# Kernel tuning notes

Hardware: AMD Instinct MI355X
Metric: run time of the kernel (lower is better)

The kernel has to match this reference:

```python
import jax, jax.numpy as jnp
import numpy as np

DIM = 1024
NUM_HEADS = 16
HEAD_DIM = DIM // NUM_HEADS
SCALE = HEAD_DIM ** -0.5
B, N = 4, 2048


def setup_inputs() -> dict:
    key = jax.random.key(0)
    ks = jax.random.split(key, 5)
    s = 1.0 / np.sqrt(DIM)  # ~ torch Linear init scale
    x = jax.random.normal(ks[0], (B, N, DIM), dtype=jnp.float32)
    Wq = jax.random.normal(ks[1], (DIM, DIM), dtype=jnp.float32) * s
    Wk = jax.random.normal(ks[2], (DIM, DIM), dtype=jnp.float32) * s
    Wv = jax.random.normal(ks[3], (DIM, DIM), dtype=jnp.float32) * s
    Wo = jax.random.normal(ks[4], (DIM, DIM), dtype=jnp.float32) * s
    mask = jnp.tril(jnp.ones((N, N), dtype=bool))  # causal 2D bool mask
    return {"x": x, "mask": mask, "Wq": Wq, "Wk": Wk, "Wv": Wv, "Wo": Wo}


def reference(x, mask, Wq, Wk, Wv, Wo):
    Bb, Nn, D = x.shape
    def split_heads(t):
        return t.reshape(Bb, Nn, NUM_HEADS, HEAD_DIM).transpose(0, 2, 1, 3)  # [B,H,N,d]
    q = split_heads(x @ Wq.T)
    k = split_heads(x @ Wk.T)
    v = split_heads(x @ Wv.T)
    attn = jnp.einsum('bhqd,bhkd->bhqk', q, k) * SCALE  # [B,H,N,N]
    # 2D mask -> broadcast over batch and heads; ~mask positions set to -inf
    attn = jnp.where(mask[None, None, :, :], attn, -jnp.inf)
    attn = jax.nn.softmax(attn, axis=-1)
    out = jnp.einsum('bhqk,bhkd->bhqd', attn, v)
    out = out.transpose(0, 2, 1, 3).reshape(Bb, Nn, D)
    return out @ Wo.T
```

## Files before the change

### kernel.cpp

```cpp
#include <hip/hip_runtime.h>
#include <stdint.h>

#define Bq   4
#define Nseq 2048
#define NH   16
#define HD   64
#define DIMD 1024

typedef float  f32x4   __attribute__((ext_vector_type(4)));
typedef float  f32x16  __attribute__((ext_vector_type(16)));
typedef __bf16 bf16x8  __attribute__((ext_vector_type(8)));
typedef short  s16x4   __attribute__((ext_vector_type(4)));

typedef __attribute__((address_space(1))) void as1_void;
typedef __attribute__((address_space(3))) void as3_void;

static __device__ __forceinline__ uint16_t f2bf(float f) {
    uint32_t u = __builtin_bit_cast(uint32_t, f);
    u += 0x7fffu + ((u >> 16) & 1u);
    return (uint16_t)(u >> 16);
}

static __device__ __forceinline__ uint32_t pk2(float a, float b) {
    uint32_t ua = __builtin_bit_cast(uint32_t, a);
    uint32_t ub = __builtin_bit_cast(uint32_t, b);
    return (ua >> 16) | (ub & 0xffff0000u);
}

static __device__ __forceinline__ void asyncLoad16(const uint16_t* g, uint16_t* l) {
    __builtin_amdgcn_global_load_lds((as1_void*)g, (as3_void*)l, 16, 0, 0);
}

static __device__ __forceinline__ void storeOut(float* p, float v)    { *p = v; }
static __device__ __forceinline__ void storeOut(uint16_t* p, float v) { *p = f2bf(v); }

__global__ void cast_all(const float* __restrict__ x,
                         const float* __restrict__ wq, const float* __restrict__ wk,
                         const float* __restrict__ wv, const float* __restrict__ wo,
                         uint16_t* __restrict__ dst) {
    size_t i = ((size_t)blockIdx.x * blockDim.x + threadIdx.x) * 4;
    const float* src; size_t off; float scale = 1.0f;
    if (i < 8388608) { src = x; off = i; }
    else {
        size_t wI = i - 8388608;
        size_t wi = wI >> 20;
        off = wI & 1048575;
        src = (wi == 0) ? wq : (wi == 1) ? wk : (wi == 2) ? wv : wo;
        if (wi == 0) scale = 0.18033688011112042f;
    }
    float4 v = *(const float4*)(src + off);
    ushort4 o;
    o.x = f2bf(v.x * scale); o.y = f2bf(v.y * scale);
    o.z = f2bf(v.z * scale); o.w = f2bf(v.w * scale);
    *(ushort4*)(dst + i) = o;
}

template <typename OutT>
__global__ __launch_bounds__(256) void gemm_bt(
    const uint16_t* __restrict__ A, const uint16_t* __restrict__ W0,
    OutT* __restrict__ C0, int K, int Nld, int blocksPerSec,
    size_t wSecStride, size_t cSecStride, uint16_t* __restrict__ vtb, int vSec)
{
    __shared__ __align__(16) uint16_t As[128*64];
    __shared__ __align__(16) uint16_t Bs[128*64];

    const int t = threadIdx.x, lane = t & 63, w = t >> 6;
    const int wr = w >> 1, wc = w & 1;
    const int half = lane >> 5, ml = lane & 31;

    const int m0  = blockIdx.x * 128;
    const int sec = blockIdx.y / blocksPerSec;
    const int n0  = (blockIdx.y % blocksPerSec) * 128;
    const uint16_t* Wp = W0 + (size_t)sec * wSecStride;
    OutT* C = C0 + (size_t)sec * cSecStride;

    int srow[4], sg[4];
    #pragma unroll
    for (int i = 0; i < 4; ++i) {
        int s = t + 256*i;
        srow[i] = s >> 3;
        sg[i]   = (s & 7) ^ (srow[i] & 7);
    }

    int arow[2], brow[2];
    #pragma unroll
    for (int i = 0; i < 2; ++i) {
        arow[i] = wr*64 + i*32 + ml;
        brow[i] = wc*64 + i*32 + ml;
    }

    f32x16 acc[2][2] = {};

    for (int k0 = 0; k0 < K; k0 += 64) {
        __syncthreads();
        #pragma unroll
        for (int i = 0; i < 4; ++i) {
            asyncLoad16(A  + (size_t)(m0 + srow[i])*K + k0 + sg[i]*8,
                        As + (size_t)(w*64 + 256*i)*8);
            asyncLoad16(Wp + (size_t)(n0 + srow[i])*K + k0 + sg[i]*8,
                        Bs + (size_t)(w*64 + 256*i)*8);
        }
        __syncthreads();

        #pragma unroll
        for (int s = 0; s < 4; ++s) {
            const int chunk = s*2 + half;
            bf16x8 af[2], bfr[2];
            #pragma unroll
            for (int i = 0; i < 2; ++i) {
                int m = arow[i];
                af[i]  = *(const bf16x8*)(As + (size_t)(m*8 + (chunk ^ (m & 7)))*8);
                int n = brow[i];
                bfr[i] = *(const bf16x8*)(Bs + (size_t)(n*8 + (chunk ^ (n & 7)))*8);
            }
            #pragma unroll
            for (int mt = 0; mt < 2; ++mt)
                #pragma unroll
                for (int nt = 0; nt < 2; ++nt)
                    acc[mt][nt] = __builtin_amdgcn_mfma_f32_32x32x16_bf16(
                        af[mt], bfr[nt], acc[mt][nt], 0, 0, 0);
        }
    }

    if (vtb != nullptr && sec == vSec) {
        #pragma unroll
        for (int mt = 0; mt < 2; ++mt)
            #pragma unroll
            for (int nt = 0; nt < 2; ++nt) {
                int colg = n0 + wc*64 + nt*32 + ml;
                int hh = colg >> 6, dd = colg & 63;
                #pragma unroll
                for (int g = 0; g < 4; ++g) {
                    int rowg = m0 + wr*64 + mt*32 + 8*g + 4*half;
                    int bb = rowg >> 11, nn = rowg & 2047;
                    ushort4 o4;
                    o4.x = f2bf(acc[mt][nt][4*g + 0]);
                    o4.y = f2bf(acc[mt][nt][4*g + 1]);
                    o4.z = f2bf(acc[mt][nt][4*g + 2]);
                    o4.w = f2bf(acc[mt][nt][4*g + 3]);
                    *(ushort4*)(vtb + ((size_t)((bb*NH + hh)*HD + dd))*Nseq + nn) = o4;
                }
            }
    } else {
        #pragma unroll
        for (int mt = 0; mt < 2; ++mt)
            #pragma unroll
            for (int nt = 0; nt < 2; ++nt) {
                int col = n0 + wc*64 + nt*32 + ml;
                #pragma unroll
                for (int r = 0; r < 16; ++r) {
                    int row = m0 + wr*64 + mt*32 + (r & 3) + 8*(r >> 2) + 4*half;
                    storeOut(&C[(size_t)row * Nld + col], acc[mt][nt][r]);
                }
            }
    }
}

__global__ __launch_bounds__(256, 4) void attn(
    const uint16_t* __restrict__ Q, const uint16_t* __restrict__ K,
    const uint16_t* __restrict__ Vt, uint16_t* __restrict__ O)
{
    __shared__ __align__(16) uint16_t Kb[2][64*64];
    __shared__ __align__(16) uint16_t Vb[2][64*64];

    const int t = threadIdx.x, lane = t & 63, w = t >> 6;
    const int quad = lane >> 4, c = lane & 15;
    const int y = blockIdx.y;
    const int qi = (y < 4) ? (15 - y) : (y < 8) ? (y + 4) : (y < 12) ? (y - 4) : (15 - y);
    const int q0 = qi * 128;
    const int bh = blockIdx.x, b = bh >> 4, h = bh & 15;
    const size_t tokBase = (size_t)b * Nseq;
    const int hcol = h * HD;
    uint16_t* Qs = (uint16_t*)Kb;

    #define STAGE_KV(k0_, buf_)                                             \
        _Pragma("unroll")                                                    \
        for (int i = 0; i < 2; ++i) {                                        \
            int s = t + 256*i;                                               \
            int row = s >> 3, gg = (s & 7) ^ (row & 7);                      \
            asyncLoad16(K + (tokBase + (k0_) + row)*DIMD + hcol + gg*8,      \
                        Kb[buf_] + (size_t)(w*64 + 256*i)*8);                \
            asyncLoad16(Vt + ((size_t)bh*HD + row)*Nseq + (k0_) + gg*8,      \
                        Vb[buf_] + (size_t)(w*64 + 256*i)*8);                \
        }

    #pragma unroll
    for (int i = 0; i < 4; ++i) {
        int s = t + 256*i;
        int row = s >> 3, gg = (s & 7) ^ (row & 7);
        asyncLoad16(Q + (tokBase + q0 + row)*DIMD + hcol + gg*8,
                    Qs + (size_t)(w*64 + 256*i)*8);
    }
    __syncthreads();
    bf16x8 qf[2][2];
    #pragma unroll
    for (int qt = 0; qt < 2; ++qt)
        #pragma unroll
        for (int ks = 0; ks < 2; ++ks) {
            int row = w*32 + qt*16 + c;
            int pos = (ks*4 + quad) ^ (row & 7);
            qf[qt][ks] = *(const bf16x8*)(Qs + (size_t)(row*8 + pos)*8);
        }
    __syncthreads();
    STAGE_KV(0, 0);

    const int wrow0 = q0 + w*32;
    const int end = 2*qi + 2;
    f32x4  o[2][4] = {};
    float  l_lane[2] = {0.f, 0.f};

    for (int kt = 0; kt < end; ++kt) {
        const int cur = kt & 1, nxt = cur ^ 1;
        const int k0 = kt * 64;
        __syncthreads();

        if (kt + 1 < end) { STAGE_KV((kt+1)*64, nxt); }

        if (k0 > wrow0 + 31) continue;

        const uint16_t* Ks = Kb[cur];
        const uint16_t* Vs = Vb[cur];

        f32x4 sv[2][4] = {};
        #pragma unroll
        for (int nt = 0; nt < 4; ++nt)
            #pragma unroll
            for (int ks = 0; ks < 2; ++ks) {
                int row = nt*16 + c;
                int pos = (ks*4 + quad) ^ (row & 7);
                bf16x8 kf = *(const bf16x8*)(Ks + (size_t)(row*8 + pos)*8);
                sv[0][nt] = __builtin_amdgcn_mfma_f32_16x16x32_bf16(kf, qf[0][ks], sv[0][nt], 0, 0, 0);
                sv[1][nt] = __builtin_amdgcn_mfma_f32_16x16x32_bf16(kf, qf[1][ks], sv[1][nt], 0, 0, 0);
            }

        if (k0 + 63 > wrow0) {
            #pragma unroll
            for (int qt = 0; qt < 2; ++qt)
                #pragma unroll
                for (int nt = 0; nt < 4; ++nt)
                    #pragma unroll
                    for (int r = 0; r < 4; ++r) {
                        int kvg = k0 + nt*16 + quad*4 + r;
                        int qg  = wrow0 + qt*16 + c;
                        if (kvg > qg) sv[qt][nt][r] = -340.0f;
                    }
        }

        s16x4 pb[2][4];
        #pragma unroll
        for (int qt = 0; qt < 2; ++qt)
            #pragma unroll
            for (int nt = 0; nt < 4; ++nt) {
                float p0 = __builtin_amdgcn_exp2f(sv[qt][nt][0]);
                float p1 = __builtin_amdgcn_exp2f(sv[qt][nt][1]);
                float p2 = __builtin_amdgcn_exp2f(sv[qt][nt][2]);
                float p3 = __builtin_amdgcn_exp2f(sv[qt][nt][3]);
                l_lane[qt] += (p0 + p1) + (p2 + p3);
                union { uint32_t u[2]; s16x4 v; } pu;
                pu.u[0] = pk2(p0, p1);
                pu.u[1] = pk2(p2, p3);
                pb[qt][nt] = pu.v;
            }

        #pragma unroll
        for (int s4 = 0; s4 < 4; ++s4)
            #pragma unroll
            for (int dt = 0; dt < 4; ++dt) {
                int row = dt*16 + c;
                int chunk = s4*2 + (quad >> 1);
                int pos = chunk ^ (row & 7);
                s16x4 vf = *(const s16x4*)(Vs + (size_t)(row*8 + pos)*8 + (quad & 1)*4);
                o[0][dt] = __builtin_amdgcn_mfma_f32_16x16x16bf16_1k(vf, pb[0][s4], o[0][dt], 0, 0, 0);
                o[1][dt] = __builtin_amdgcn_mfma_f32_16x16x16bf16_1k(vf, pb[1][s4], o[1][dt], 0, 0, 0);
            }
    }

    #pragma unroll
    for (int qt = 0; qt < 2; ++qt) {
        float l = l_lane[qt];
        l += __shfl_xor(l, 16);
        l += __shfl_xor(l, 32);
        float inv = 1.0f / l;
        int tok = (int)(q0 + w*32 + qt*16 + c);
        #pragma unroll
        for (int dt = 0; dt < 4; ++dt) {
            ushort4 o4;
            o4.x = f2bf(o[qt][dt][0] * inv);
            o4.y = f2bf(o[qt][dt][1] * inv);
            o4.z = f2bf(o[qt][dt][2] * inv);
            o4.w = f2bf(o[qt][dt][3] * inv);
            *(ushort4*)(O + (tokBase + tok)*DIMD + hcol + dt*16 + quad*4) = o4;
        }
    }
    #undef STAGE_KV
}

extern "C" void kernel_launch(void* const* d_in, const int* in_sizes, int n_in,
                              void* d_out, int out_size, void* d_ws, size_t ws_size,
                              hipStream_t stream) {
    const float* x  = (const float*)d_in[0];
    const float* Wq = (const float*)d_in[2];
    const float* Wk = (const float*)d_in[3];
    const float* Wv = (const float*)d_in[4];
    const float* Wo = (const float*)d_in[5];

    uint16_t* ws  = (uint16_t*)d_ws;
    uint16_t* xb  = ws;
    uint16_t* wqb = ws + 8388608;
    uint16_t* wob = wqb + 3*1048576;
    uint16_t* qb  = ws + 12582912;
    uint16_t* kb  = qb + 8388608;
    uint16_t* vtb = kb + 8388608;
    uint16_t* ab  = xb;

    cast_all<<<12288, 256, 0, stream>>>(x, Wq, Wk, Wv, Wo, ws);

    gemm_bt<uint16_t><<<dim3(64, 24), 256, 0, stream>>>(
        xb, wqb, qb, DIMD, DIMD, 8, (size_t)1048576, (size_t)8388608, vtb, 2);

    attn<<<dim3(64, 16), 256, 0, stream>>>(qb, kb, vtb, ab);

    gemm_bt<float><<<dim3(64, 8), 256, 0, stream>>>(
        ab, wob, (float*)d_out, DIMD, DIMD, 8, (size_t)0, (size_t)0, nullptr, -1);
}
```

Before: 248.4 us.

## Add 256x256-tile double-buffered QKV GEMM with interleaved async prefetch

Replaces the 128x128 QKV projection GEMM with a new 512-thread kernel that computes 256x256 output tiles. It double-buffers A and B in LDS with async global-to-LDS loads spread between MFMA phases, and uses explicit barriers and s_setprio to overlap loads with compute. The larger tile raises arithmetic intensity and cuts global traffic, but the kernel uses 128KB of LDS and launches only 384 blocks, so occupancy and tail balance are at risk. The V section still writes a transposed layout, now as ushort4 stores.

```diff
diff --git a/kernel.cpp b/kernel.cpp
--- a/kernel.cpp
+++ b/kernel.cpp
@@ -55,6 +55,152 @@
     *(ushort4*)(dst + i) = o;
 }
 
+#define BAR()    asm volatile("s_barrier" ::: "memory")
+#define VMBAR(N) asm volatile("s_waitcnt vmcnt(" #N ")\n\ts_barrier" ::: "memory")
+
+__global__ __launch_bounds__(512, 2) void gemm256_qkv(
+    const uint16_t* __restrict__ A, const uint16_t* __restrict__ W0,
+    uint16_t* __restrict__ C0, uint16_t* __restrict__ vtb)
+{
+    __shared__ __align__(16) uint16_t As[2][16384];
+    __shared__ __align__(16) uint16_t Bs[2][16384];
+
+    const int t = threadIdx.x, lane = t & 63, w = t >> 6;
+    const int wm = w >> 2, wn = w & 3;
+    const int ml = lane & 31, half = lane >> 5;
+
+    const int m0  = blockIdx.x * 256;
+    const int sec = blockIdx.y >> 2;
+    const int n0  = (blockIdx.y & 3) * 256;
+    const uint16_t* __restrict__ Wp = W0 + (size_t)sec * 1048576;
+
+    const int srow = t >> 3;
+    const int sg   = (t & 7) ^ (srow & 7);
+    const size_t aOff = (size_t)(m0 + srow) * DIMD + sg * 8;
+    const size_t bOff = (size_t)(n0 + srow) * DIMD + sg * 8;
+    const int slot = w * 512;
+
+#define SA(set_, buf_, kk_) asyncLoad16(A  + aOff + (size_t)(set_)*64*DIMD + (kk_), \
+                                        &As[buf_][(set_)*4096 + slot])
+#define SB(set_, buf_, kk_) asyncLoad16(Wp + bOff + (size_t)(set_)*64*DIMD + (kk_), \
+                                        &Bs[buf_][(set_)*4096 + slot])
+
+    SB(0,0,0); SB(1,0,0); SB(2,0,0); SB(3,0,0);
+    SA(0,0,0); SA(2,0,0);
+    SA(1,0,0); SA(3,0,0);
+    VMBAR(2);
+
+    int pos8[4];
+    #pragma unroll
+    for (int s = 0; s < 4; ++s) pos8[s] = ((s*2 + half) ^ (ml & 7)) * 8;
+    const int arow0 = (wm*128 + ml) * 64;
+    const int brow0 = (wn*64  + ml) * 64;
+
+    f32x16 acc[4][2] = {};
+
+    #pragma unroll 2
+    for (int kt = 0; kt < 16; ++kt) {
+        const int cur = kt & 1, nxt = cur ^ 1;
+        const int k1 = (kt + 1) * 64;
+        const bool pf = (kt + 1 < 16);
+        const uint16_t* __restrict__ Ac = As[cur];
+        const uint16_t* __restrict__ Bc = Bs[cur];
+
+        bf16x8 af[2][4], bf[2][4];
+
+        #pragma unroll
+        for (int i = 0; i < 2; ++i)
+            #pragma unroll
+            for (int s = 0; s < 4; ++s) {
+                af[i][s] = *(const bf16x8*)(Ac + arow0 + i*2048 + pos8[s]);
+                bf[i][s] = *(const bf16x8*)(Bc + brow0 + i*2048 + pos8[s]);
+            }
+        if (pf) { SB(0,nxt,k1); SB(1,nxt,k1); }
+        BAR();
+        __builtin_amdgcn_s_setprio(1);
+        #pragma unroll
+        for (int s = 0; s < 4; ++s) {
+            acc[0][0] = __builtin_amdgcn_mfma_f32_32x32x16_bf16(af[0][s], bf[0][s], acc[0][0], 0,0,0);
+            acc[1][0] = __builtin_amdgcn_mfma_f32_32x32x16_bf16(af[1][s], bf[0][s], acc[1][0], 0,0,0);
+        }
+        __builtin_amdgcn_s_setprio(0);
+        BAR();
+
+        if (pf) { SB(2,nxt,k1); SB(3,nxt,k1); SA(0,nxt,k1); SA(2,nxt,k1); }
+        BAR();
+        __builtin_amdgcn_s_setprio(1);
+        #pragma unroll
+        for (int s = 0; s < 4; ++s) {
+            acc[0][1] = __builtin_amdgcn_mfma_f32_32x32x16_bf16(af[0][s], bf[1][s], acc[0][1], 0,0,0);
+            acc[1][1] = __builtin_amdgcn_mfma_f32_32x32x16_bf16(af[1][s], bf[1][s], acc[1][1], 0,0,0);
+        }
+        __builtin_amdgcn_s_setprio(0);
+        if (pf) { VMBAR(6); } else { VMBAR(0); }
+
+        #pragma unroll
+        for (int i = 0; i < 2; ++i)
+            #pragma unroll
+            for (int s = 0; s < 4; ++s)
+                af[i][s] = *(const bf16x8*)(Ac + arow0 + 4096 + i*2048 + pos8[s]);
+        if (pf) { SA(1,nxt,k1); SA(3,nxt,k1); }
+        BAR();
+        __builtin_amdgcn_s_setprio(1);
+        #pragma unroll
+        for (int s = 0; s < 4; ++s) {
+            acc[2][0] = __builtin_amdgcn_mfma_f32_32x32x16_bf16(af[0][s], bf[0][s], acc[2][0], 0,0,0);
+            acc[3][0] = __builtin_amdgcn_mfma_f32_32x32x16_bf16(af[1][s], bf[0][s], acc[3][0], 0,0,0);
+        }
+        __builtin_amdgcn_s_setprio(0);
+        BAR();
+
+        __builtin_amdgcn_s_setprio(1);
+        #pragma unroll
+        for (int s = 0; s < 4; ++s) {
+            acc[2][1] = __builtin_amdgcn_mfma_f32_32x32x16_bf16(af[0][s], bf[1][s], acc[2][1], 0,0,0);
+            acc[3][1] = __builtin_amdgcn_mfma_f32_32x32x16_bf16(af[1][s], bf[1][s], acc[3][1], 0,0,0);
+        }
+        __builtin_amdgcn_s_setprio(0);
+        if (pf) { VMBAR(2); } else { BAR(); }
+    }
+
+#undef SA
+#undef SB
+
+    if (sec == 2) {
+        #pragma unroll
+        for (int mt = 0; mt < 4; ++mt)
+            #pragma unroll
+            for (int nt = 0; nt < 2; ++nt) {
+                int colg = n0 + wn*64 + nt*32 + ml;
+                int hh = colg >> 6, dd = colg & 63;
+                #pragma unroll
+                for (int g = 0; g < 4; ++g) {
+                    int rowg = m0 + wm*128 + mt*32 + 8*g + 4*half;
+                    int bb = rowg >> 11, nn = rowg & 2047;
+                    ushort4 o4;
+                    o4.x = f2bf(acc[mt][nt][4*g + 0]);
+                    o4.y = f2bf(acc[mt][nt][4*g + 1]);
+                    o4.z = f2bf(acc[mt][nt][4*g + 2]);
+                    o4.w = f2bf(acc[mt][nt][4*g + 3]);
+                    *(ushort4*)(vtb + ((size_t)((bb*NH + hh)*HD + dd))*Nseq + nn) = o4;
+                }
+            }
+    } else {
+        uint16_t* C = C0 + (size_t)sec * 8388608;
+        #pragma unroll
+        for (int mt = 0; mt < 4; ++mt)
+            #pragma unroll
+            for (int nt = 0; nt < 2; ++nt) {
+                int col = n0 + wn*64 + nt*32 + ml;
+                #pragma unroll
+                for (int r = 0; r < 16; ++r) {
+                    int row = m0 + wm*128 + mt*32 + (r & 3) + 8*(r >> 2) + 4*half;
+                    C[(size_t)row * DIMD + col] = f2bf(acc[mt][nt][r]);
+                }
+            }
+    }
+}
+
 template <typename OutT>
 __global__ __launch_bounds__(256) void gemm_bt(
     const uint16_t* __restrict__ A, const uint16_t* __restrict__ W0,
@@ -315,8 +461,7 @@
 
     cast_all<<<12288, 256, 0, stream>>>(x, Wq, Wk, Wv, Wo, ws);
 
-    gemm_bt<uint16_t><<<dim3(64, 24), 256, 0, stream>>>(
-        xb, wqb, qb, DIMD, DIMD, 8, (size_t)1048576, (size_t)8388608, vtb, 2);
+    gemm256_qkv<<<dim3(32, 12), 512, 0, stream>>>(xb, wqb, qb, vtb);
 
     attn<<<dim3(64, 16), 256, 0, stream>>>(qb, kb, vtb, ab);
 
```

Measured after the change: 261.3 us. 5.2% more time.

## Use 16x16x32 MFMA for PV via cross-lane P shuffle and add setprio

Applied to the files above, without the earlier changes.

The P·V product switches from the 16x16x16 bf16 MFMA to the 16x16x32 variant. To build the 8-element bf16 P fragments it needs, the code permutes packed P values across lanes with two xor shuffles. V is loaded from shared memory as 16-byte vectors instead of 8-byte ones. This halves the number of MFMA issues and LDS reads for the PV step, at the cost of extra shuffles and selects. It also raises wave priority around both MFMA blocks so matrix work is favored over other waves' exp and softmax work.

```diff
diff --git a/kernel.cpp b/kernel.cpp
--- a/kernel.cpp
+++ b/kernel.cpp
@@ -165,6 +165,8 @@
 
     const int t = threadIdx.x, lane = t & 63, w = t >> 6;
     const int quad = lane >> 4, c = lane & 15;
+    const bool lo = (lane < 32);
+    const bool edge = (quad == 0) || (quad == 3);
     const int y = blockIdx.y;
     const int qi = (y < 4) ? (15 - y) : (y < 8) ? (y + 4) : (y < 12) ? (y - 4) : (15 - y);
     const int q0 = qi * 128;
@@ -222,6 +224,7 @@
         const uint16_t* Vs = Vb[cur];
 
         f32x4 sv[2][4] = {};
+        __builtin_amdgcn_s_setprio(1);
         #pragma unroll
         for (int nt = 0; nt < 4; ++nt)
             #pragma unroll
@@ -232,6 +235,7 @@
                 sv[0][nt] = __builtin_amdgcn_mfma_f32_16x16x32_bf16(kf, qf[0][ks], sv[0][nt], 0, 0, 0);
                 sv[1][nt] = __builtin_amdgcn_mfma_f32_16x16x32_bf16(kf, qf[1][ks], sv[1][nt], 0, 0, 0);
             }
+        __builtin_amdgcn_s_setprio(0);
 
         if (k0 + 63 > wrow0) {
             #pragma unroll
@@ -246,33 +250,50 @@
                     }
         }
 
-        s16x4 pb[2][4];
+        bf16x8 pbig[2][2];
         #pragma unroll
         for (int qt = 0; qt < 2; ++qt)
             #pragma unroll
-            for (int nt = 0; nt < 4; ++nt) {
-                float p0 = __builtin_amdgcn_exp2f(sv[qt][nt][0]);
-                float p1 = __builtin_amdgcn_exp2f(sv[qt][nt][1]);
-                float p2 = __builtin_amdgcn_exp2f(sv[qt][nt][2]);
-                float p3 = __builtin_amdgcn_exp2f(sv[qt][nt][3]);
-                l_lane[qt] += (p0 + p1) + (p2 + p3);
-                union { uint32_t u[2]; s16x4 v; } pu;
-                pu.u[0] = pk2(p0, p1);
-                pu.u[1] = pk2(p2, p3);
-                pb[qt][nt] = pu.v;
-            }
-
-        #pragma unroll
-        for (int s4 = 0; s4 < 4; ++s4)
+            for (int pair = 0; pair < 2; ++pair) {
+                uint32_t eo[4];
+                #pragma unroll
+                for (int hf = 0; hf < 2; ++hf) {
+                    int nt = pair*2 + hf;
+                    float p0 = __builtin_amdgcn_exp2f(sv[qt][nt][0]);
+                    float p1 = __builtin_amdgcn_exp2f(sv[qt][nt][1]);
+                    float p2 = __builtin_amdgcn_exp2f(sv[qt][nt][2]);
+                    float p3 = __builtin_amdgcn_exp2f(sv[qt][nt][3]);
+                    l_lane[qt] += (p0 + p1) + (p2 + p3);
+                    eo[hf*2 + 0] = pk2(p0, p1);
+                    eo[hf*2 + 1] = pk2(p2, p3);
+                }
+                union { uint32_t u[4]; bf16x8 v; } pw;
+                #pragma unroll
+                for (int x = 0; x < 2; ++x) {
+                    uint32_t E = eo[x], Ov = eo[2 + x];
+                    uint32_t send1 = lo ? Ov : E;
+                    uint32_t r1 = __shfl_xor(send1, 32);
+                    uint32_t comp = lo ? E : Ov;
+                    uint32_t send2 = edge ? r1 : comp;
+                    uint32_t r2 = __shfl_xor(send2, 16);
+                    pw.u[x]     = (quad == 0) ? E  : (quad == 2) ? r1 : r2;
+                    pw.u[2 + x] = (quad == 3) ? Ov : (quad == 1) ? r1 : r2;
+                }
+                pbig[qt][pair] = pw.v;
+            }
+
+        __builtin_amdgcn_s_setprio(1);
+        #pragma unroll
+        for (int pair = 0; pair < 2; ++pair)
             #pragma unroll
             for (int dt = 0; dt < 4; ++dt) {
                 int row = dt*16 + c;
-                int chunk = s4*2 + (quad >> 1);
-                int pos = chunk ^ (row & 7);
-                s16x4 vf = *(const s16x4*)(Vs + (size_t)(row*8 + pos)*8 + (quad & 1)*4);
-                o[0][dt] = __builtin_amdgcn_mfma_f32_16x16x16bf16_1k(vf, pb[0][s4], o[0][dt], 0, 0, 0);
-                o[1][dt] = __builtin_amdgcn_mfma_f32_16x16x16bf16_1k(vf, pb[1][s4], o[1][dt], 0, 0, 0);
-            }
+                int pos = (pair*4 + quad) ^ (row & 7);
+                bf16x8 vf = *(const bf16x8*)(Vs + (size_t)(row*8 + pos)*8);
+                o[0][dt] = __builtin_amdgcn_mfma_f32_16x16x32_bf16(vf, pbig[0][pair], o[0][dt], 0, 0, 0);
+                o[1][dt] = __builtin_amdgcn_mfma_f32_16x16x32_bf16(vf, pbig[1][pair], o[1][dt], 0, 0, 0);
+            }
+        __builtin_amdgcn_s_setprio(0);
     }
 
     #pragma unroll
```

After: 272.8 us. 1.1x slower.
